# Kernel optimization log

Measured on AMD Instinct MI355X. Metric: run time of the kernel, lower is better.

Reference implementation:

```python
import jax, jax.numpy as jnp
import numpy as np

FP8_MAX = 448.0
EPS = 1e-12


def setup_inputs() -> dict:
    key = jax.random.key(0)
    k1, k2 = jax.random.split(key)
    x = jax.random.normal(k1, (4, 2048, 4096), dtype=jnp.float32)
    # kaiming-uniform-like init scale for weight
    weight = jax.random.normal(k2, (4096, 4096), dtype=jnp.float32) * 0.02
    bias = jnp.zeros((4096,), dtype=jnp.float32)
    return {"x": x, "weight": weight, "bias": bias}


def reference(x, weight, bias):
    # per-tensor fake-quant of activations
    input_scale = jnp.maximum(jnp.max(jnp.abs(x)) / FP8_MAX, EPS)
    x_q = jnp.round(jnp.clip(x / input_scale, -FP8_MAX, FP8_MAX))
    # per-tensor fake-quant of weight
    weight_scale = jnp.maximum(jnp.max(jnp.abs(weight)) / FP8_MAX, EPS)
    weight_q = jnp.round(jnp.clip(weight / weight_scale, -FP8_MAX, FP8_MAX))
    # GEMM in quantized domain, then dequant rescale + bias
    out_q = jnp.einsum('bsi,oi->bso', x_q, weight_q)  # [B,S,out]
    out = (out_q * (input_scale * weight_scale)).astype(x.dtype) + bias
    return out
```

## Files before the change

### kernel.cpp

```cpp
#include <hip/hip_runtime.h>

#define FP8_MAX 448.0f
#define EPSF 1e-12f

#define BM 256
#define BN 256
#define BK 32

typedef __attribute__((ext_vector_type(8))) _Float16 half8;
typedef __attribute__((ext_vector_type(4))) float floatx4;

#define VMCNT(n) asm volatile("s_waitcnt vmcnt(" #n ")" ::: "memory")

__device__ inline void async_copy16(const void* gp, void* lp) {
  __builtin_amdgcn_global_load_lds(
      (const __attribute__((address_space(1))) unsigned int*)gp,
      (__attribute__((address_space(3))) unsigned int*)lp,
      16, 0, 0);
}

__global__ void absmax2_kernel(const float* __restrict__ a, int n4a,
                               const float* __restrict__ b, int n4b,
                               int blocks_a, unsigned* __restrict__ out) {
  const bool isA = (int)blockIdx.x < blocks_a;
  const float4* in4 = (const float4*)(isA ? a : b);
  const int n4 = isA ? n4a : n4b;
  const int nblk = isA ? blocks_a : (gridDim.x - blocks_a);
  const int bid = isA ? blockIdx.x : (blockIdx.x - blocks_a);
  int tid = bid * blockDim.x + threadIdx.x;
  int stride = nblk * blockDim.x;
  float m = 0.f;
  for (int i = tid; i < n4; i += stride) {
    float4 v = in4[i];
    m = fmaxf(m, fmaxf(fmaxf(fabsf(v.x), fabsf(v.y)),
                       fmaxf(fabsf(v.z), fabsf(v.w))));
  }
  for (int off = 32; off > 0; off >>= 1)
    m = fmaxf(m, __shfl_down(m, off, 64));
  __shared__ float smax[4];
  int lane = threadIdx.x & 63, w = threadIdx.x >> 6;
  if (lane == 0) smax[w] = m;
  __syncthreads();
  if (threadIdx.x == 0) {
    float bm = fmaxf(fmaxf(smax[0], smax[1]), fmaxf(smax[2], smax[3]));
    atomicMax(out + (isA ? 0 : 1), __float_as_uint(bm));
  }
}

__global__ void quant2_kernel(const float* __restrict__ a, int n8a,
                              const float* __restrict__ b, int n8b,
                              int blocks_a, _Float16* __restrict__ qa,
                              _Float16* __restrict__ qb,
                              const unsigned* __restrict__ amax_bits) {
  const bool isA = (int)blockIdx.x < blocks_a;
  const float4* in4 = (const float4*)(isA ? a : b);
  half8* out8 = (half8*)(isA ? qa : qb);
  const int n8 = isA ? n8a : n8b;
  const int nblk = isA ? blocks_a : (gridDim.x - blocks_a);
  const int bid = isA ? blockIdx.x : (blockIdx.x - blocks_a);
  const float scale =
      fmaxf(__uint_as_float(amax_bits[isA ? 0 : 1]) / FP8_MAX, EPSF);
  int tid = bid * blockDim.x + threadIdx.x;
  int stride = nblk * blockDim.x;
  for (int i = tid; i < n8; i += stride) {
    float4 va = in4[2 * i], vb = in4[2 * i + 1];
    half8 h;
    h[0] = (_Float16)rintf(fminf(fmaxf(va.x / scale, -FP8_MAX), FP8_MAX));
    h[1] = (_Float16)rintf(fminf(fmaxf(va.y / scale, -FP8_MAX), FP8_MAX));
    h[2] = (_Float16)rintf(fminf(fmaxf(va.z / scale, -FP8_MAX), FP8_MAX));
    h[3] = (_Float16)rintf(fminf(fmaxf(va.w / scale, -FP8_MAX), FP8_MAX));
    h[4] = (_Float16)rintf(fminf(fmaxf(vb.x / scale, -FP8_MAX), FP8_MAX));
    h[5] = (_Float16)rintf(fminf(fmaxf(vb.y / scale, -FP8_MAX), FP8_MAX));
    h[6] = (_Float16)rintf(fminf(fmaxf(vb.z / scale, -FP8_MAX), FP8_MAX));
    h[7] = (_Float16)rintf(fminf(fmaxf(vb.w / scale, -FP8_MAX), FP8_MAX));
    out8[i] = h;
  }
}

__global__ __launch_bounds__(512, 1) void gemm8_kernel(
    const _Float16* __restrict__ A,
    const _Float16* __restrict__ B,
    const float* __restrict__ bias, const unsigned* __restrict__ amax,
    float* __restrict__ C,
    int M, int N, int K) {
  __shared__ __align__(16) _Float16 As[4][BM * BK];
  __shared__ __align__(16) _Float16 Bs[4][BN * BK];

  const int tid = threadIdx.x;
  const int w = tid >> 6;
  const int lane = tid & 63;
  const int wr = w >> 2;
  const int wc = w & 3;

  const int nwg = gridDim.x;
  const int cpx = nwg >> 3;
  const int swz = (blockIdx.x & 7) * cpx + (blockIdx.x >> 3);
  const int nbn = N / BN;
  const int bm = swz / nbn;
  const int bn = swz % nbn;

  const _Float16* Ab = A + (size_t)bm * BM * K;
  const _Float16* Bb = B + (size_t)bn * BN * K;

  const int gd8 = ((lane & 3) ^ ((lane >> 3) & 3)) * 8;
  const _Float16* Ag = Ab + (size_t)(lane >> 2) * K + gd8;
  const _Float16* Bg = Bb + (size_t)(lane >> 2) * K + gd8;

  auto stage = [&](int kt) {
#pragma unroll
    for (int r = 0; r < 2; ++r) {
      const int R0 = r * 128 + w * 16;
      async_copy16(Ag + (size_t)R0 * K + kt * BK,
                   (void*)&As[kt & 3][R0 * BK]);
    }
#pragma unroll
    for (int r = 0; r < 2; ++r) {
      const int R0 = r * 128 + w * 16;
      async_copy16(Bg + (size_t)R0 * K + kt * BK,
                   (void*)&Bs[kt & 3][R0 * BK]);
    }
  };

  const int lr = lane & 15;
  const int hi = lane >> 4;
  const int gsw = (hi ^ ((lr >> 1) & 3)) * 8;
  const int aoff = (wr * 128 + lr) * BK + gsw;
  const int boff = (wc * 64 + lr) * BK + gsw;

  half8 afA[8], bfA[4], afB[8], bfB[4];
  floatx4 acc[8][4] = {};
  const int nt = K / BK;

  auto readFrags = [&](int kt, half8 (&af)[8], half8 (&bf)[4]) {
    const _Float16* Asb = &As[kt & 3][0];
    const _Float16* Bsb = &Bs[kt & 3][0];
#pragma unroll
    for (int m = 0; m < 8; ++m)
      af[m] = *(const half8*)&Asb[aoff + m * 16 * BK];
#pragma unroll
    for (int n = 0; n < 4; ++n)
      bf[n] = *(const half8*)&Bsb[boff + n * 16 * BK];
  };

  auto mfmaAll = [&](half8 (&af)[8], half8 (&bf)[4]) {
    __builtin_amdgcn_s_setprio(1);
#pragma unroll
    for (int m = 0; m < 8; ++m)
#pragma unroll
      for (int n = 0; n < 4; ++n)
        acc[m][n] = __builtin_amdgcn_mfma_f32_16x16x32_f16(
            af[m], bf[n], acc[m][n], 0, 0, 0);
    __builtin_amdgcn_s_setprio(0);
  };

  stage(0); stage(1); stage(2);
  VMCNT(4);
  __builtin_amdgcn_s_barrier();
  readFrags(0, afA, bfA);

  for (int t = 0; t < nt; t += 2) {
    if (t + 1 < nt) readFrags(t + 1, afB, bfB);
    if (t + 3 < nt) stage(t + 3);
    mfmaAll(afA, bfA);
    if (t + 3 < nt) { VMCNT(4); } else { VMCNT(0); }
    __builtin_amdgcn_s_barrier();

    if (t + 2 < nt) readFrags(t + 2, afA, bfA);
    if (t + 4 < nt) stage(t + 4);
    mfmaAll(afB, bfB);
    if (t + 4 < nt) { VMCNT(4); } else { VMCNT(0); }
    __builtin_amdgcn_s_barrier();
  }

  const float sx = fmaxf(__uint_as_float(amax[0]) / FP8_MAX, EPSF);
  const float sw = fmaxf(__uint_as_float(amax[1]) / FP8_MAX, EPSF);
  const float s = sx * sw;

  const int row0 = bm * BM + wr * 128 + hi * 4;
  const int col0 = bn * BN + wc * 64 + lr;
  float bv[4];
#pragma unroll
  for (int n = 0; n < 4; ++n) bv[n] = bias[col0 + n * 16];

#pragma unroll
  for (int m = 0; m < 8; ++m) {
#pragma unroll
    for (int n = 0; n < 4; ++n) {
      const size_t base = (size_t)(row0 + m * 16) * N + col0 + n * 16;
#pragma unroll
      for (int r = 0; r < 4; ++r)
        C[base + (size_t)r * N] = acc[m][n][r] * s + bv[n];
    }
  }
}

extern "C" void kernel_launch(void* const* d_in, const int* in_sizes, int n_in,
                              void* d_out, int out_size, void* d_ws,
                              size_t ws_size, hipStream_t stream) {
  const float* x = (const float*)d_in[0];
  const float* wgt = (const float*)d_in[1];
  const float* bias = (const float*)d_in[2];
  float* out = (float*)d_out;

  const int N = in_sizes[2];
  const int K = in_sizes[1] / N;
  const int M = in_sizes[0] / K;

  unsigned* amax = (unsigned*)d_ws;
  _Float16* xq = (_Float16*)((char*)d_ws + 256);
  _Float16* wq =
      (_Float16*)((char*)d_ws + 256 + (size_t)M * K * sizeof(_Float16));

  hipMemsetAsync(d_ws, 0, 8, stream);
  absmax2_kernel<<<3072, 256, 0, stream>>>(x, M * K / 4, wgt, N * K / 4, 2048,
                                           amax);
  quant2_kernel<<<3072, 256, 0, stream>>>(x, M * K / 8, wgt, N * K / 8, 2048,
                                          xq, wq, amax);

  gemm8_kernel<<<dim3((M / BM) * (N / BN)), 512, 0, stream>>>(
      xq, wq, bias, amax, out, M, N, K);
}
```

Before: 351.2 us.

## Load B fragments directly from global memory into registers, bypassing LDS

The B (weight) operand is no longer staged through shared memory. Each wave loads its own B fragments straight from global memory into registers one k-tile ahead, and only A keeps the 4-stage LDS pipeline. The block-to-tile mapping also changes: groups of 8 consecutive blocks now cover 8 column tiles for the same row tile, which is meant to improve L2 reuse of the weight tiles. This halves LDS traffic and footprint, at the cost of redundant global loads of B across the two wave rows, uncoalesced 16-byte per-lane loads, and vmcnt accounting that mixes direct loads with async LDS copies.

Result: slower. 516.4 us (+47.0%).

```diff
diff --git a/kernel.cpp b/kernel.cpp
--- a/kernel.cpp
+++ b/kernel.cpp
@@ -84,7 +84,6 @@
     float* __restrict__ C,
     int M, int N, int K) {
   __shared__ __align__(16) _Float16 As[4][BM * BK];
-  __shared__ __align__(16) _Float16 Bs[4][BN * BK];
 
   const int tid = threadIdx.x;
   const int w = tid >> 6;
@@ -92,83 +91,81 @@
   const int wr = w >> 2;
   const int wc = w & 3;
 
-  const int nwg = gridDim.x;
-  const int cpx = nwg >> 3;
-  const int swz = (blockIdx.x & 7) * cpx + (blockIdx.x >> 3);
-  const int nbn = N / BN;
-  const int bm = swz / nbn;
-  const int bn = swz % nbn;
+  const int nbm = M / BM;
+  const int bm = (blockIdx.x >> 3) % nbm;
+  const int bn = (blockIdx.x & 7) + 8 * ((blockIdx.x >> 3) / nbm);
 
   const _Float16* Ab = A + (size_t)bm * BM * K;
-  const _Float16* Bb = B + (size_t)bn * BN * K;
 
   const int gd8 = ((lane & 3) ^ ((lane >> 3) & 3)) * 8;
   const _Float16* Ag = Ab + (size_t)(lane >> 2) * K + gd8;
-  const _Float16* Bg = Bb + (size_t)(lane >> 2) * K + gd8;
-
-  auto stage = [&](int kt) {
+
+  auto stageA = [&](int kt) {
 #pragma unroll
     for (int r = 0; r < 2; ++r) {
       const int R0 = r * 128 + w * 16;
       async_copy16(Ag + (size_t)R0 * K + kt * BK,
                    (void*)&As[kt & 3][R0 * BK]);
     }
-#pragma unroll
-    for (int r = 0; r < 2; ++r) {
-      const int R0 = r * 128 + w * 16;
-      async_copy16(Bg + (size_t)R0 * K + kt * BK,
-                   (void*)&Bs[kt & 3][R0 * BK]);
-    }
   };
 
   const int lr = lane & 15;
   const int hi = lane >> 4;
   const int gsw = (hi ^ ((lr >> 1) & 3)) * 8;
   const int aoff = (wr * 128 + lr) * BK + gsw;
-  const int boff = (wc * 64 + lr) * BK + gsw;
-
-  half8 afA[8], bfA[4], afB[8], bfB[4];
+
+  const _Float16* Bgf = B + (size_t)(bn * BN + wc * 64 + lr) * K + hi * 8;
+
+  half8 afA[8], afB[8], bgA[4], bgB[4];
   floatx4 acc[8][4] = {};
   const int nt = K / BK;
 
-  auto readFrags = [&](int kt, half8 (&af)[8], half8 (&bf)[4]) {
+  auto readFrags = [&](int kt, half8 (&af)[8]) {
     const _Float16* Asb = &As[kt & 3][0];
-    const _Float16* Bsb = &Bs[kt & 3][0];
 #pragma unroll
     for (int m = 0; m < 8; ++m)
       af[m] = *(const half8*)&Asb[aoff + m * 16 * BK];
+  };
+  auto loadB = [&](int kt, half8 (&bg)[4]) {
 #pragma unroll
     for (int n = 0; n < 4; ++n)
-      bf[n] = *(const half8*)&Bsb[boff + n * 16 * BK];
-  };
-
-  auto mfmaAll = [&](half8 (&af)[8], half8 (&bf)[4]) {
+      bg[n] = *(const half8*)(Bgf + (size_t)(n * 16) * K + (size_t)kt * BK);
+  };
+  auto mfmaAll = [&](half8 (&af)[8], half8 (&bg)[4]) {
     __builtin_amdgcn_s_setprio(1);
 #pragma unroll
     for (int m = 0; m < 8; ++m)
 #pragma unroll
       for (int n = 0; n < 4; ++n)
         acc[m][n] = __builtin_amdgcn_mfma_f32_16x16x32_f16(
-            af[m], bf[n], acc[m][n], 0, 0, 0);
+            af[m], bg[n], acc[m][n], 0, 0, 0);
     __builtin_amdgcn_s_setprio(0);
   };
 
-  stage(0); stage(1); stage(2);
-  VMCNT(4);
+  stageA(0); stageA(1);
+  loadB(0, bgA);
+  stageA(2);
+  VMCNT(2);
   __builtin_amdgcn_s_barrier();
-  readFrags(0, afA, bfA);
+  readFrags(0, afA);
 
   for (int t = 0; t < nt; t += 2) {
-    if (t + 1 < nt) readFrags(t + 1, afB, bfB);
-    if (t + 3 < nt) stage(t + 3);
-    mfmaAll(afA, bfA);
-    if (t + 3 < nt) { VMCNT(4); } else { VMCNT(0); }
+    if (t + 1 < nt) { loadB(t + 1, bgB); readFrags(t + 1, afB); }
+    if (t + 3 < nt) stageA(t + 3);
+    __builtin_amdgcn_sched_barrier(0);
+    mfmaAll(afA, bgA);
+    if (t + 3 < nt) { VMCNT(6); }
+    else if (t + 1 < nt) { VMCNT(4); }
+    else { VMCNT(0); }
     __builtin_amdgcn_s_barrier();
 
-    if (t + 2 < nt) readFrags(t + 2, afA, bfA);
-    if (t + 4 < nt) stage(t + 4);
-    mfmaAll(afB, bfB);
-    if (t + 4 < nt) { VMCNT(4); } else { VMCNT(0); }
+    if (t + 2 < nt) { loadB(t + 2, bgA); readFrags(t + 2, afA); }
+    if (t + 4 < nt) stageA(t + 4);
+    __builtin_amdgcn_sched_barrier(0);
+    mfmaAll(afB, bgB);
+    if (t + 4 < nt) { VMCNT(6); }
+    else if (t + 2 < nt) { VMCNT(4); }
+    else { VMCNT(0); }
     __builtin_amdgcn_s_barrier();
   }
 
```
